# Performance work log

Measured on AMD Instinct MI355X. Metric: run time of the kernel, lower is better.

Reference implementation:

```python
import jax, jax.numpy as jnp
import numpy as np

NEG_INF = -jnp.inf  # aggregation identity for the max-plus semifield


def setup_inputs() -> dict:
    key = jax.random.key(0)
    k1, k2, k3 = jax.random.split(key, 3)
    B, C_in, C_out, H, W, M, N = 4, 32, 32, 80, 80, 5, 5
    x = jax.random.normal(k1, (B, C_in, H, W), dtype=jnp.float32)
    w = jax.random.normal(k2, (C_out, C_in, M, N), dtype=jnp.float32) * 0.1
    bias = jax.random.normal(k3, (C_out,), dtype=jnp.float32) * 0.1
    return {"x": x, "w": w, "bias": bias}


def reference(x, w, bias):
    """Max-plus semifield conv: out[b,co,h,w] = bias[co] + sum_ci max_{m,n} (x_pad[b,ci,h+m,w+n] + w[co,ci,m,n]).

    Faithful to SemiConv2d._semi_conv with semifield = (amax, add, -inf, 0),
    but computed with a running max over the MN taps instead of materializing
    the [B, C_out, C_in, M*N, H*W] tensor the torch code builds via unfold.
    """
    B, C_in, H, W = x.shape
    C_out, _, M, N = w.shape
    # padding exactly as in _semi_conv (odd vs even kernel), fill = aggregation identity
    pt, pb = (M // 2, M // 2) if M % 2 else (M // 2 - 1, M // 2)
    pl, pr = (N // 2, N // 2) if N % 2 else (N // 2 - 1, N // 2)
    xp = jnp.pad(x, ((0, 0), (0, 0), (pt, pb), (pl, pr)), constant_values=NEG_INF)
    # running max over the M*N taps (fixed small loop, not a data-dim loop)
    acc = jnp.full((B, C_out, C_in, H, W), NEG_INF, dtype=x.dtype)
    for m in range(M):
        for n in range(N):
            patch = xp[:, :, m:m + H, n:n + W]               # [B, C_in, H, W]
            tap = patch[:, None] + w[None, :, :, m, n, None, None]  # [B, C_out, C_in, H, W]
            acc = jnp.maximum(acc, tap)
    out = jnp.sum(acc, axis=2) + bias[None, :, None, None]   # sum over C_in, add bias
    return out
```

## Files before the change

### kernel.cpp

```cpp
#include <hip/hip_runtime.h>
#include <math.h>

#define CIN  32
#define COUT 32
#define BB   4
#define HH   80
#define WW   80
#define HW   (HH * WW)
#define NOUT (BB * COUT * HW)
#define TH   16
#define XR   (TH + 4)
#define XC   (WW + 4)
#define TILE (XR * XC)
#define NT   320

template<int NPARTS>
__global__ __launch_bounds__(NT, 4) void semiconv_kernel(
    const float* __restrict__ x,
    const float* __restrict__ w,
    const float* __restrict__ bias,
    float* __restrict__ dst)
{
    constexpr int CIP = CIN / NPARTS;
    __shared__ __align__(16) float xs[2][TILE];

    const int tid = threadIdx.x;
    const int bh  = blockIdx.x;
    const int cp  = blockIdx.y;
    const int zz  = blockIdx.z;
    const int b    = zz / NPARTS;
    const int part = zz % NPARTS;
    const int ci0  = part * CIP;
    const int h0   = bh * TH;
    const int co0  = cp * 2;

    const int ty = tid / 20;
    const int tx = tid % 20;
    const int wc = tx * 4;

    int goff[6];
    #pragma unroll
    for (int i = 0; i < 6; ++i) {
        int idx = tid + i * NT;
        int r = idx / XC, c = idx % XC;
        int gr = h0 + r - 2, gc = c - 2;
        goff[i] = (gr >= 0 && gr < HH && gc >= 0 && gc < WW) ? (gr * WW + gc) : -1;
    }
    const bool has6 = (tid < TILE - 5 * NT);

    float pre[6];
    auto prefetch = [&](int ci) {
        const float* xp = x + (size_t)(b * CIN + ci) * HW;
        #pragma unroll
        for (int i = 0; i < 5; ++i)
            pre[i] = (goff[i] >= 0) ? xp[goff[i]] : -INFINITY;
        if (has6) pre[5] = (goff[5] >= 0) ? xp[goff[5]] : -INFINITY;
    };

    const float* wp0 = w + ((size_t)(co0    ) * CIN + ci0) * 25;
    const float* wp1 = w + ((size_t)(co0 + 1) * CIN + ci0) * 25;

    prefetch(ci0);
    float s0a=0.f,s1a=0.f,s2a=0.f,s3a=0.f;
    float s0b=0.f,s1b=0.f,s2b=0.f,s3b=0.f;
    int buf = 0;

    for (int k = 0; k < CIP; ++k) {
        float w0[25], w1[25];
        #pragma unroll
        for (int j = 0; j < 25; ++j) { w0[j] = wp0[k * 25 + j]; w1[j] = wp1[k * 25 + j]; }

        float* xb = xs[buf];
        #pragma unroll
        for (int i = 0; i < 5; ++i) xb[tid + i * NT] = pre[i];
        if (has6) xb[tid + 5 * NT] = pre[5];
        __syncthreads();
        if (k + 1 < CIP) prefetch(ci0 + k + 1);

        float a0=-INFINITY,a1=-INFINITY,a2=-INFINITY,a3=-INFINITY;
        float b0=-INFINITY,b1=-INFINITY,b2=-INFINITY,b3=-INFINITY;
        #pragma unroll
        for (int m = 0; m < 5; ++m) {
            const float4* rp = reinterpret_cast<const float4*>(&xb[(ty + m) * XC + wc]);
            float4 A = rp[0], C = rp[1];
            float x0=A.x,x1=A.y,x2=A.z,x3=A.w,x4=C.x,x5=C.y,x6=C.z,x7=C.w;
            {
                float q0=w0[5*m],q1=w0[5*m+1],q2=w0[5*m+2],q3=w0[5*m+3],q4=w0[5*m+4];
                float t, u;
                t=fmaxf(fmaxf(x0+q0,x1+q1),x2+q2); u=fmaxf(x3+q3,x4+q4); a0=fmaxf(fmaxf(a0,t),u);
                t=fmaxf(fmaxf(x1+q0,x2+q1),x3+q2); u=fmaxf(x4+q3,x5+q4); a1=fmaxf(fmaxf(a1,t),u);
                t=fmaxf(fmaxf(x2+q0,x3+q1),x4+q2); u=fmaxf(x5+q3,x6+q4); a2=fmaxf(fmaxf(a2,t),u);
                t=fmaxf(fmaxf(x3+q0,x4+q1),x5+q2); u=fmaxf(x6+q3,x7+q4); a3=fmaxf(fmaxf(a3,t),u);
            }
            {
                float q0=w1[5*m],q1=w1[5*m+1],q2=w1[5*m+2],q3=w1[5*m+3],q4=w1[5*m+4];
                float t, u;
                t=fmaxf(fmaxf(x0+q0,x1+q1),x2+q2); u=fmaxf(x3+q3,x4+q4); b0=fmaxf(fmaxf(b0,t),u);
                t=fmaxf(fmaxf(x1+q0,x2+q1),x3+q2); u=fmaxf(x4+q3,x5+q4); b1=fmaxf(fmaxf(b1,t),u);
                t=fmaxf(fmaxf(x2+q0,x3+q1),x4+q2); u=fmaxf(x5+q3,x6+q4); b2=fmaxf(fmaxf(b2,t),u);
                t=fmaxf(fmaxf(x3+q0,x4+q1),x5+q2); u=fmaxf(x6+q3,x7+q4); b3=fmaxf(fmaxf(b3,t),u);
            }
        }
        s0a+=a0; s1a+=a1; s2a+=a2; s3a+=a3;
        s0b+=b0; s1b+=b1; s2b+=b2; s3b+=b3;
        buf ^= 1;
    }

    size_t oiA = (((size_t)b * COUT + co0    ) * HH + (h0 + ty)) * WW + wc;
    size_t oiB = (((size_t)b * COUT + co0 + 1) * HH + (h0 + ty)) * WW + wc;
    float4 rA, rB;
    if (NPARTS == 1) {
        const float bcA = bias[co0], bcB = bias[co0 + 1];
        rA.x=s0a+bcA; rA.y=s1a+bcA; rA.z=s2a+bcA; rA.w=s3a+bcA;
        rB.x=s0b+bcB; rB.y=s1b+bcB; rB.z=s2b+bcB; rB.w=s3b+bcB;
    } else {
        rA.x=s0a; rA.y=s1a; rA.z=s2a; rA.w=s3a;
        rB.x=s0b; rB.y=s1b; rB.z=s2b; rB.w=s3b;
        oiA += (size_t)part * NOUT;
        oiB += (size_t)part * NOUT;
    }
    *reinterpret_cast<float4*>(dst + oiA) = rA;
    *reinterpret_cast<float4*>(dst + oiB) = rB;
}

template<int NPARTS>
__global__ __launch_bounds__(256) void reduceN_kernel(
    const float* __restrict__ ws, const float* __restrict__ bias,
    float* __restrict__ out)
{
    int i4 = blockIdx.x * 256 + threadIdx.x;
    const float4* p = reinterpret_cast<const float4*>(ws);
    float4 r = p[i4];
    #pragma unroll
    for (int q = 1; q < NPARTS; ++q) {
        float4 t = p[i4 + (size_t)q * (NOUT / 4)];
        r.x += t.x; r.y += t.y; r.z += t.z; r.w += t.w;
    }
    int co = (i4 / (HW / 4)) & (COUT - 1);
    float bc = bias[co];
    r.x += bc; r.y += bc; r.z += bc; r.w += bc;
    reinterpret_cast<float4*>(out)[i4] = r;
}

extern "C" void kernel_launch(void* const* d_in, const int* in_sizes, int n_in,
                              void* d_out, int out_size, void* d_ws, size_t ws_size,
                              hipStream_t stream) {
    const float* x    = (const float*)d_in[0];
    const float* w    = (const float*)d_in[1];
    const float* bias = (const float*)d_in[2];
    float* out        = (float*)d_out;

    const size_t need4 = 4ull * NOUT * sizeof(float);
    const size_t need2 = 2ull * NOUT * sizeof(float);

    if (ws_size >= need4) {
        dim3 grid(HH / TH, COUT / 2, BB * 4);
        semiconv_kernel<4><<<grid, NT, 0, stream>>>(x, w, bias, (float*)d_ws);
        reduceN_kernel<4><<<NOUT / 4 / 256, 256, 0, stream>>>((const float*)d_ws, bias, out);
    } else if (ws_size >= need2) {
        dim3 grid(HH / TH, COUT / 2, BB * 2);
        semiconv_kernel<2><<<grid, NT, 0, stream>>>(x, w, bias, (float*)d_ws);
        reduceN_kernel<2><<<NOUT / 4 / 256, 256, 0, stream>>>((const float*)d_ws, bias, out);
    } else {
        dim3 grid(HH / TH, COUT / 2, BB);
        semiconv_kernel<1><<<grid, NT, 0, stream>>>(x, w, bias, out);
    }
}
```

Before: 42.63 us.

## Stream input tiles directly to LDS, stage weights in LDS, use v_max3

Replaces the register-staged prefetch of input tiles with global_load_lds direct-to-LDS asynchronous copies into two ping-pong buffers, with padding cells filled once with -inf. Weights for both output channels are preloaded into LDS in an interleaved layout and read as vectors instead of per-iteration scalar global loads. The max reductions use inline v_max3_f32, and launch bounds rise to 7 blocks per CU. The aim is to cut VGPR pressure and global-load latency in the inner loop; the risk is correctness of the wave-relative LDS addressing for the direct loads and whether the compiler orders those async copies correctly against __syncthreads.

```diff
diff --git a/kernel.cpp b/kernel.cpp
--- a/kernel.cpp
+++ b/kernel.cpp
@@ -9,34 +9,56 @@
 #define HW   (HH * WW)
 #define NOUT (BB * COUT * HW)
 #define TH   16
-#define XR   (TH + 4)
-#define XC   (WW + 4)
-#define TILE (XR * XC)
+#define XR   20
+#define XC   84
+#define TILE 1680
 #define NT   320
 
-template<int NPARTS>
-__global__ __launch_bounds__(NT, 4) void semiconv_kernel(
+typedef float v4f __attribute__((ext_vector_type(4)));
+
+__device__ __forceinline__ float max3f(float a, float b, float c) {
+    float d;
+    asm("v_max3_f32 %0, %1, %2, %3" : "=v"(d) : "v"(a), "v"(b), "v"(c));
+    return d;
+}
+
+__device__ __forceinline__ void load_lds4(const float* g, float* l) {
+    __builtin_amdgcn_global_load_lds(
+        (const __attribute__((address_space(1))) void*)g,
+        (__attribute__((address_space(3))) void*)l, 4, 0, 0);
+}
+
+template<int NP>
+__global__ __launch_bounds__(NT, 7) void semiconv_kernel(
     const float* __restrict__ x,
     const float* __restrict__ w,
     const float* __restrict__ bias,
     float* __restrict__ dst)
 {
-    constexpr int CIP = CIN / NPARTS;
-    __shared__ __align__(16) float xs[2][TILE];
+    constexpr int CP = CIN / NP;
+    __shared__ __align__(16) float xs0[TILE];
+    __shared__ __align__(16) float xs1[TILE];
+    __shared__ __align__(16) float wl[CP * 60];
 
     const int tid = threadIdx.x;
     const int bh  = blockIdx.x;
     const int cp  = blockIdx.y;
     const int zz  = blockIdx.z;
-    const int b    = zz / NPARTS;
-    const int part = zz % NPARTS;
-    const int ci0  = part * CIP;
+    const int b    = zz / NP;
+    const int part = zz % NP;
+    const int ci0  = part * CP;
     const int h0   = bh * TH;
     const int co0  = cp * 2;
 
-    const int ty = tid / 20;
-    const int tx = tid % 20;
-    const int wc = tx * 4;
+    for (int idx = tid; idx < CP * 60; idx += NT) {
+        int k = idx / 60, r = idx % 60, m = r / 12, q = r % 12;
+        float v = 0.f;
+        if (q < 10)
+            v = w[((size_t)(co0 + (q & 1)) * CIN + ci0 + k) * 25 + m * 5 + (q >> 1)];
+        wl[idx] = v;
+    }
+
+    const int ty = tid / 20, tx = tid % 20, wc = tx * 4;
 
     int goff[6];
     #pragma unroll
@@ -44,86 +66,82 @@
         int idx = tid + i * NT;
         int r = idx / XC, c = idx % XC;
         int gr = h0 + r - 2, gc = c - 2;
-        goff[i] = (gr >= 0 && gr < HH && gc >= 0 && gc < WW) ? (gr * WW + gc) : -1;
+        bool in = (idx < TILE) && gr >= 0 && gr < HH && gc >= 0 && gc < WW;
+        goff[i] = in ? (gr * WW + gc) : -1;
+        if (idx < TILE && !in) { xs0[idx] = -INFINITY; xs1[idx] = -INFINITY; }
     }
-    const bool has6 = (tid < TILE - 5 * NT);
 
-    float pre[6];
-    auto prefetch = [&](int ci) {
-        const float* xp = x + (size_t)(b * CIN + ci) * HW;
+    const float* xbase = x + (size_t)(b * CIN + ci0) * HW;
+    const int wave64 = tid & ~63;
+
+    #pragma unroll
+    for (int i = 0; i < 6; ++i)
+        if (goff[i] >= 0) load_lds4(xbase + goff[i], xs0 + i * NT + wave64);
+
+    const float* xnext = xbase + HW;
+    float sA[4] = {0.f, 0.f, 0.f, 0.f}, sB[4] = {0.f, 0.f, 0.f, 0.f};
+    const int xro = ty * XC + wc;
+
+    __syncthreads();
+
+    auto step = [&](int k, const float* xrd, float* xwr) {
+        if (k + 1 < CP) {
+            #pragma unroll
+            for (int i = 0; i < 6; ++i)
+                if (goff[i] >= 0) load_lds4(xnext + goff[i], xwr + i * NT + wave64);
+            xnext += HW;
+        }
+        const float* wk = &wl[k * 60];
+        float aA[4] = {-INFINITY, -INFINITY, -INFINITY, -INFINITY};
+        float aB[4] = {-INFINITY, -INFINITY, -INFINITY, -INFINITY};
         #pragma unroll
-        for (int i = 0; i < 5; ++i)
-            pre[i] = (goff[i] >= 0) ? xp[goff[i]] : -INFINITY;
-        if (has6) pre[5] = (goff[5] >= 0) ? xp[goff[5]] : -INFINITY;
+        for (int m = 0; m < 5; ++m) {
+            v4f A  = *(const v4f*)(xrd + xro + m * XC);
+            v4f C  = *(const v4f*)(xrd + xro + m * XC + 4);
+            v4f W0 = *(const v4f*)(wk + m * 12);
+            v4f W1 = *(const v4f*)(wk + m * 12 + 4);
+            v4f W2 = *(const v4f*)(wk + m * 12 + 8);
+            float xr[8] = {A.x, A.y, A.z, A.w, C.x, C.y, C.z, C.w};
+            float wa[5] = {W0.x, W0.z, W1.x, W1.z, W2.x};
+            float wb[5] = {W0.y, W0.w, W1.y, W1.w, W2.y};
+            #pragma unroll
+            for (int j = 0; j < 4; ++j) {
+                float p0 = xr[j] + wa[0], p1 = xr[j+1] + wa[1], p2 = xr[j+2] + wa[2];
+                float p3 = xr[j+3] + wa[3], p4 = xr[j+4] + wa[4];
+                aA[j] = max3f(aA[j], max3f(p0, p1, p2), fmaxf(p3, p4));
+                p0 = xr[j] + wb[0]; p1 = xr[j+1] + wb[1]; p2 = xr[j+2] + wb[2];
+                p3 = xr[j+3] + wb[3]; p4 = xr[j+4] + wb[4];
+                aB[j] = max3f(aB[j], max3f(p0, p1, p2), fmaxf(p3, p4));
+            }
+        }
+        #pragma unroll
+        for (int j = 0; j < 4; ++j) { sA[j] += aA[j]; sB[j] += aB[j]; }
+        __syncthreads();
     };
 
-    const float* wp0 = w + ((size_t)(co0    ) * CIN + ci0) * 25;
-    const float* wp1 = w + ((size_t)(co0 + 1) * CIN + ci0) * 25;
-
-    prefetch(ci0);
-    float s0a=0.f,s1a=0.f,s2a=0.f,s3a=0.f;
-    float s0b=0.f,s1b=0.f,s2b=0.f,s3b=0.f;
-    int buf = 0;
-
-    for (int k = 0; k < CIP; ++k) {
-        float w0[25], w1[25];
-        #pragma unroll
-        for (int j = 0; j < 25; ++j) { w0[j] = wp0[k * 25 + j]; w1[j] = wp1[k * 25 + j]; }
-
-        float* xb = xs[buf];
-        #pragma unroll
-        for (int i = 0; i < 5; ++i) xb[tid + i * NT] = pre[i];
-        if (has6) xb[tid + 5 * NT] = pre[5];
-        __syncthreads();
-        if (k + 1 < CIP) prefetch(ci0 + k + 1);
-
-        float a0=-INFINITY,a1=-INFINITY,a2=-INFINITY,a3=-INFINITY;
-        float b0=-INFINITY,b1=-INFINITY,b2=-INFINITY,b3=-INFINITY;
-        #pragma unroll
-        for (int m = 0; m < 5; ++m) {
-            const float4* rp = reinterpret_cast<const float4*>(&xb[(ty + m) * XC + wc]);
-            float4 A = rp[0], C = rp[1];
-            float x0=A.x,x1=A.y,x2=A.z,x3=A.w,x4=C.x,x5=C.y,x6=C.z,x7=C.w;
-            {
-                float q0=w0[5*m],q1=w0[5*m+1],q2=w0[5*m+2],q3=w0[5*m+3],q4=w0[5*m+4];
-                float t, u;
-                t=fmaxf(fmaxf(x0+q0,x1+q1),x2+q2); u=fmaxf(x3+q3,x4+q4); a0=fmaxf(fmaxf(a0,t),u);
-                t=fmaxf(fmaxf(x1+q0,x2+q1),x3+q2); u=fmaxf(x4+q3,x5+q4); a1=fmaxf(fmaxf(a1,t),u);
-                t=fmaxf(fmaxf(x2+q0,x3+q1),x4+q2); u=fmaxf(x5+q3,x6+q4); a2=fmaxf(fmaxf(a2,t),u);
-                t=fmaxf(fmaxf(x3+q0,x4+q1),x5+q2); u=fmaxf(x6+q3,x7+q4); a3=fmaxf(fmaxf(a3,t),u);
-            }
-            {
-                float q0=w1[5*m],q1=w1[5*m+1],q2=w1[5*m+2],q3=w1[5*m+3],q4=w1[5*m+4];
-                float t, u;
-                t=fmaxf(fmaxf(x0+q0,x1+q1),x2+q2); u=fmaxf(x3+q3,x4+q4); b0=fmaxf(fmaxf(b0,t),u);
-                t=fmaxf(fmaxf(x1+q0,x2+q1),x3+q2); u=fmaxf(x4+q3,x5+q4); b1=fmaxf(fmaxf(b1,t),u);
-                t=fmaxf(fmaxf(x2+q0,x3+q1),x4+q2); u=fmaxf(x5+q3,x6+q4); b2=fmaxf(fmaxf(b2,t),u);
-                t=fmaxf(fmaxf(x3+q0,x4+q1),x5+q2); u=fmaxf(x6+q3,x7+q4); b3=fmaxf(fmaxf(b3,t),u);
-            }
-        }
-        s0a+=a0; s1a+=a1; s2a+=a2; s3a+=a3;
-        s0b+=b0; s1b+=b1; s2b+=b2; s3b+=b3;
-        buf ^= 1;
+    #pragma unroll 1
+    for (int k = 0; k < CP; k += 2) {
+        step(k,     xs0, xs1);
+        step(k + 1, xs1, xs0);
     }
 
-    size_t oiA = (((size_t)b * COUT + co0    ) * HH + (h0 + ty)) * WW + wc;
-    size_t oiB = (((size_t)b * COUT + co0 + 1) * HH + (h0 + ty)) * WW + wc;
-    float4 rA, rB;
-    if (NPARTS == 1) {
-        const float bcA = bias[co0], bcB = bias[co0 + 1];
-        rA.x=s0a+bcA; rA.y=s1a+bcA; rA.z=s2a+bcA; rA.w=s3a+bcA;
-        rB.x=s0b+bcB; rB.y=s1b+bcB; rB.z=s2b+bcB; rB.w=s3b+bcB;
+    size_t oiA = (((size_t)b * COUT + co0) * HH + (h0 + ty)) * WW + wc;
+    size_t oiB = oiA + (size_t)HW;
+    v4f rA = {sA[0], sA[1], sA[2], sA[3]};
+    v4f rB = {sB[0], sB[1], sB[2], sB[3]};
+    float* o = dst;
+    if (NP == 1) {
+        float bcA = bias[co0], bcB = bias[co0 + 1];
+        rA.x += bcA; rA.y += bcA; rA.z += bcA; rA.w += bcA;
+        rB.x += bcB; rB.y += bcB; rB.z += bcB; rB.w += bcB;
     } else {
-        rA.x=s0a; rA.y=s1a; rA.z=s2a; rA.w=s3a;
-        rB.x=s0b; rB.y=s1b; rB.z=s2b; rB.w=s3b;
-        oiA += (size_t)part * NOUT;
-        oiB += (size_t)part * NOUT;
+        o += (size_t)part * NOUT;
     }
-    *reinterpret_cast<float4*>(dst + oiA) = rA;
-    *reinterpret_cast<float4*>(dst + oiB) = rB;
+    *(v4f*)(o + oiA) = rA;
+    *(v4f*)(o + oiB) = rB;
 }
 
-template<int NPARTS>
+template<int NP>
 __global__ __launch_bounds__(256) void reduceN_kernel(
     const float* __restrict__ ws, const float* __restrict__ bias,
     float* __restrict__ out)
@@ -132,7 +150,7 @@
     const float4* p = reinterpret_cast<const float4*>(ws);
     float4 r = p[i4];
     #pragma unroll
-    for (int q = 1; q < NPARTS; ++q) {
+    for (int q = 1; q < NP; ++q) {
         float4 t = p[i4 + (size_t)q * (NOUT / 4)];
         r.x += t.x; r.y += t.y; r.z += t.z; r.w += t.w;
     }
```

Result: faster. 38.19 us (-10.4%).
